# Kernel optimization log

Hardware: AMD Instinct MI355X
Metric: run time of the kernel (lower is better)

## Reference

```python
import jax, jax.numpy as jnp
import numpy as np

BATCH = 32768


def _unpack(packed, n):
    # packed: [rows, ceil(n/8)] ints in [0,256). Extract bits MSB-first per byte.
    bits = (packed[:, :, None] >> jnp.arange(7, -1, -1, dtype=packed.dtype)) & 1
    return bits.reshape(packed.shape[0], -1)[:, :n]  # [rows, n] of {0,1}


def setup_inputs() -> dict:
    key = jax.random.key(0)
    k0, k1, k2, k3, k4 = jax.random.split(key, 5)
    return {
        "x": jax.random.normal(k0, (BATCH, 784), dtype=jnp.float32),
        "w1_packed": jax.random.randint(k1, (256, 98), 0, 256, dtype=jnp.int32),
        "m1_packed": jax.random.randint(k2, (256, 98), 0, 256, dtype=jnp.int32),
        "alpha1": jnp.float32(1.0),
        "w2_packed": jax.random.randint(k3, (10, 32), 0, 256, dtype=jnp.int32),
        "m2_packed": jax.random.randint(k4, (10, 32), 0, 256, dtype=jnp.int32),
        "alpha2": jnp.float32(1.0),
    }


def reference(x, w1_packed, m1_packed, alpha1, w2_packed, m2_packed, alpha2):
    # Layer 1: binary {-1,+1} weights * {0,1} mask * alpha
    w1 = (2 * _unpack(w1_packed, 784) - 1).astype(jnp.float32)
    w1 = w1 * _unpack(m1_packed, 784).astype(jnp.float32) * alpha1  # [256, 784]
    h = jax.nn.relu(jnp.einsum('bi,oi->bo', x, w1))  # [B, 256]
    # Layer 2
    w2 = (2 * _unpack(w2_packed, 256) - 1).astype(jnp.float32)
    w2 = w2 * _unpack(m2_packed, 256).astype(jnp.float32) * alpha2  # [10, 256]
    return jnp.einsum('bh,oh->bo', h, w2)  # [B, 10]
```

## Files before the change

### kernel.cpp

```cpp
#include <hip/hip_runtime.h>
#include <hip/hip_bf16.h>

typedef __bf16 bf16x8 __attribute__((ext_vector_type(8)));
typedef float floatx4 __attribute__((ext_vector_type(4)));

#define GLB_AS __attribute__((address_space(1)))
#define LDS_AS __attribute__((address_space(3)))

__device__ __forceinline__ void async_cp16(const void* g, void* l) {
  __builtin_amdgcn_global_load_lds((GLB_AS void*)g, (LDS_AS void*)l, 16, 0, 0);
}

__device__ __forceinline__ unsigned short f2bf(float f) {
  __bf16 b = (__bf16)f;
  return __builtin_bit_cast(unsigned short, b);
}

__global__ void decode_w1_kernel(const int* __restrict__ w1p,
                                 const int* __restrict__ m1p,
                                 unsigned short* __restrict__ w1d) {
  int t = blockIdx.x * 256 + threadIdx.x;
  if (t >= 256 * 100) return;
  int r = t / 100;
  int j = t - r * 100;
  unsigned short vals[8];
#pragma unroll
  for (int k = 0; k < 8; ++k) vals[k] = 0;
  if (j < 98) {
    unsigned int v = (unsigned int)w1p[r * 98 + j];
    unsigned int m = (unsigned int)m1p[r * 98 + j];
#pragma unroll
    for (int k = 0; k < 8; ++k) {
      unsigned int bit = (v >> (7 - k)) & 1u;
      unsigned int mk  = (m >> (7 - k)) & 1u;
      vals[k] = (unsigned short)(mk ? (bit ? 0x3F80u : 0xBF80u) : 0u);
    }
  }
  uint4 pack;
  pack.x = (unsigned)vals[0] | ((unsigned)vals[1] << 16);
  pack.y = (unsigned)vals[2] | ((unsigned)vals[3] << 16);
  pack.z = (unsigned)vals[4] | ((unsigned)vals[5] << 16);
  pack.w = (unsigned)vals[6] | ((unsigned)vals[7] << 16);
  *reinterpret_cast<uint4*>(w1d + t * 8) = pack;
}

#define BM 64
#define BK 32
#define NCH 25
#define W1LD 800
#define HS_LD 264

__global__ __launch_bounds__(256, 2) void fused_kernel(
    const float* __restrict__ x,
    const unsigned short* __restrict__ w1d,
    const int* __restrict__ w2p,
    const int* __restrict__ m2p,
    const float* __restrict__ a1p,
    const float* __restrict__ a2p,
    float* __restrict__ out) {
  __shared__ unsigned short smem[64 * 264 + 16 * 256];

  const int tid  = threadIdx.x;
  const int wave = tid >> 6;
  const int lane = tid & 63;
  const int l15  = lane & 15;
  const int quad = lane >> 4;
  const int row0 = blockIdx.x * BM;

  const int OFF_XS = 0;
  const int OFF_WS = 2048;
  const int OFF_HS = 0;
  const int OFF_W2 = 16896;

  floatx4 acc[4][4];
#pragma unroll
  for (int i = 0; i < 4; ++i)
#pragma unroll
    for (int j = 0; j < 4; ++j) acc[i][j] = (floatx4){0.f, 0.f, 0.f, 0.f};

  for (int kc = 0; kc < NCH; ++kc) {
#pragma unroll
    for (int it = 0; it < 4; ++it) {
      int seg = it * 256 + tid;
      int r = seg >> 2, c = seg & 3;
      async_cp16(w1d + r * W1LD + kc * BK + c * 8, &smem[OFF_WS + seg * 8]);
    }
    float4 xv[2];
#pragma unroll
    for (int it = 0; it < 2; ++it) {
      int seg = it * 256 + tid;
      int r = seg >> 3, c4 = seg & 7;
      int col = kc * BK + c4 * 4;
      if (col < 784) {
        xv[it] = *reinterpret_cast<const float4*>(
            x + (size_t)(row0 + r) * 784 + col);
      } else {
        xv[it] = (float4){0.f, 0.f, 0.f, 0.f};
      }
    }
#pragma unroll
    for (int it = 0; it < 2; ++it) {
      int seg = it * 256 + tid;
      int r = seg >> 3, c4 = seg & 7;
      ushort4 b;
      b.x = f2bf(xv[it].x); b.y = f2bf(xv[it].y);
      b.z = f2bf(xv[it].z); b.w = f2bf(xv[it].w);
      *reinterpret_cast<ushort4*>(&smem[OFF_XS + r * BK + c4 * 4]) = b;
    }
    __syncthreads();

    bf16x8 af[4], bfr[4];
#pragma unroll
    for (int mi = 0; mi < 4; ++mi)
      af[mi] = *reinterpret_cast<const bf16x8*>(
          &smem[OFF_XS + (mi * 16 + l15) * BK + quad * 8]);
#pragma unroll
    for (int nj = 0; nj < 4; ++nj)
      bfr[nj] = *reinterpret_cast<const bf16x8*>(
          &smem[OFF_WS + (wave * 64 + nj * 16 + l15) * BK + quad * 8]);
#pragma unroll
    for (int mi = 0; mi < 4; ++mi)
#pragma unroll
      for (int nj = 0; nj < 4; ++nj)
        acc[mi][nj] = __builtin_amdgcn_mfma_f32_16x16x32_bf16(
            af[mi], bfr[nj], acc[mi][nj], 0, 0, 0);
    __syncthreads();
  }

  const float a1 = a1p[0];
  const float a2 = a2p[0];
#pragma unroll
  for (int mi = 0; mi < 4; ++mi) {
#pragma unroll
    for (int nj = 0; nj < 4; ++nj) {
      int col   = wave * 64 + nj * 16 + l15;
      int rbase = mi * 16 + quad * 4;
#pragma unroll
      for (int r = 0; r < 4; ++r) {
        float h = fmaxf(a1 * acc[mi][nj][r], 0.f);
        smem[OFF_HS + (rbase + r) * HS_LD + col] = f2bf(h);
      }
    }
  }
#pragma unroll
  for (int it = 0; it < 2; ++it) {
    int idx = it * 256 + tid;
    if (idx < 320) {
      int r = idx >> 5, j = idx & 31;
      unsigned int v = (unsigned int)w2p[r * 32 + j];
      unsigned int m = (unsigned int)m2p[r * 32 + j];
#pragma unroll
      for (int k = 0; k < 8; ++k) {
        unsigned int bit = (v >> (7 - k)) & 1u;
        unsigned int mk  = (m >> (7 - k)) & 1u;
        smem[OFF_W2 + r * 256 + j * 8 + k] =
            (unsigned short)(mk ? (bit ? 0x3F80u : 0xBF80u) : 0u);
      }
    }
  }
#pragma unroll
  for (int r = 10; r < 16; ++r) smem[OFF_W2 + r * 256 + tid] = 0;
  __syncthreads();

  floatx4 o2 = (floatx4){0.f, 0.f, 0.f, 0.f};
#pragma unroll
  for (int ks = 0; ks < 8; ++ks) {
    bf16x8 ha = *reinterpret_cast<const bf16x8*>(
        &smem[OFF_HS + (wave * 16 + l15) * HS_LD + ks * 32 + quad * 8]);
    bf16x8 wb = *reinterpret_cast<const bf16x8*>(
        &smem[OFF_W2 + l15 * 256 + ks * 32 + quad * 8]);
    o2 = __builtin_amdgcn_mfma_f32_16x16x32_bf16(ha, wb, o2, 0, 0, 0);
  }
  if (l15 < 10) {
#pragma unroll
    for (int r = 0; r < 4; ++r) {
      int gr = row0 + wave * 16 + quad * 4 + r;
      out[(size_t)gr * 10 + l15] = a2 * o2[r];
    }
  }
}

extern "C" void kernel_launch(void* const* d_in, const int* in_sizes, int n_in,
                              void* d_out, int out_size, void* d_ws, size_t ws_size,
                              hipStream_t stream) {
  const float* x   = (const float*)d_in[0];
  const int*   w1p = (const int*)d_in[1];
  const int*   m1p = (const int*)d_in[2];
  const float* a1  = (const float*)d_in[3];
  const int*   w2p = (const int*)d_in[4];
  const int*   m2p = (const int*)d_in[5];
  const float* a2  = (const float*)d_in[6];
  unsigned short* w1d = (unsigned short*)d_ws;
  float* out = (float*)d_out;

  decode_w1_kernel<<<100, 256, 0, stream>>>(w1p, m1p, w1d);
  fused_kernel<<<512, 256, 0, stream>>>(x, w1d, w2p, m2p, a1, a2, out);
}
```

Baseline: 187.5 us.

## Load MFMA fragments directly from global memory, drop LDS staging and barriers

The layer-1 GEMM no longer stages x and decoded W1 tiles through LDS with two barriers per K-chunk. Each wave now reads its A fragments (fp32 x, converted to bf16 in registers) and its B fragments (bf16 W1) straight from global memory, with x register-prefetched one chunk ahead. Waves are rearranged into a 2x2 grid, each owning 32 rows by 128 columns, so accumulators become 2x8 tiles. This removes LDS traffic and synchronisation, but W1 is re-read from global or L2 by every wave and the per-lane loads are strided, so it relies on cache hits.

```diff
diff --git a/kernel.cpp b/kernel.cpp
--- a/kernel.cpp
+++ b/kernel.cpp
@@ -3,13 +3,6 @@
 
 typedef __bf16 bf16x8 __attribute__((ext_vector_type(8)));
 typedef float floatx4 __attribute__((ext_vector_type(4)));
-
-#define GLB_AS __attribute__((address_space(1)))
-#define LDS_AS __attribute__((address_space(3)))
-
-__device__ __forceinline__ void async_cp16(const void* g, void* l) {
-  __builtin_amdgcn_global_load_lds((GLB_AS void*)g, (LDS_AS void*)l, 16, 0, 0);
-}
 
 __device__ __forceinline__ unsigned short f2bf(float f) {
   __bf16 b = (__bf16)f;
@@ -44,9 +37,6 @@
   *reinterpret_cast<uint4*>(w1d + t * 8) = pack;
 }
 
-#define BM 64
-#define BK 32
-#define NCH 25
 #define W1LD 800
 #define HS_LD 264
 
@@ -58,83 +48,96 @@
     const float* __restrict__ a1p,
     const float* __restrict__ a2p,
     float* __restrict__ out) {
-  __shared__ unsigned short smem[64 * 264 + 16 * 256];
+  __shared__ unsigned short smem[64 * HS_LD + 16 * 256];
 
   const int tid  = threadIdx.x;
   const int wave = tid >> 6;
   const int lane = tid & 63;
   const int l15  = lane & 15;
   const int quad = lane >> 4;
-  const int row0 = blockIdx.x * BM;
-
-  const int OFF_XS = 0;
-  const int OFF_WS = 2048;
+  const int wm   = wave >> 1;
+  const int wn   = wave & 1;
+  const int row0 = blockIdx.x * 64;
+
   const int OFF_HS = 0;
-  const int OFF_W2 = 16896;
-
-  floatx4 acc[4][4];
-#pragma unroll
-  for (int i = 0; i < 4; ++i)
-#pragma unroll
-    for (int j = 0; j < 4; ++j) acc[i][j] = (floatx4){0.f, 0.f, 0.f, 0.f};
-
-  for (int kc = 0; kc < NCH; ++kc) {
-#pragma unroll
-    for (int it = 0; it < 4; ++it) {
-      int seg = it * 256 + tid;
-      int r = seg >> 2, c = seg & 3;
-      async_cp16(w1d + r * W1LD + kc * BK + c * 8, &smem[OFF_WS + seg * 8]);
-    }
-    float4 xv[2];
-#pragma unroll
-    for (int it = 0; it < 2; ++it) {
-      int seg = it * 256 + tid;
-      int r = seg >> 3, c4 = seg & 7;
-      int col = kc * BK + c4 * 4;
-      if (col < 784) {
-        xv[it] = *reinterpret_cast<const float4*>(
-            x + (size_t)(row0 + r) * 784 + col);
+  const int OFF_W2 = 64 * HS_LD;
+
+  const float* xbase[2];
+#pragma unroll
+  for (int mi = 0; mi < 2; ++mi)
+    xbase[mi] = x + (size_t)(row0 + wm * 32 + mi * 16 + l15) * 784;
+  const unsigned short* wbase[8];
+#pragma unroll
+  for (int nj = 0; nj < 8; ++nj)
+    wbase[nj] = w1d + (size_t)(wn * 128 + nj * 16 + l15) * W1LD;
+
+  floatx4 acc[2][8];
+#pragma unroll
+  for (int i = 0; i < 2; ++i)
+#pragma unroll
+    for (int j = 0; j < 8; ++j) acc[i][j] = (floatx4){0.f, 0.f, 0.f, 0.f};
+
+  const float4 z4 = (float4){0.f, 0.f, 0.f, 0.f};
+
+  auto ldA = [&](int kc, float4 a[2][2]) {
+    int k = kc * 32 + quad * 8;
+    bool ok = (k < 784);
+#pragma unroll
+    for (int mi = 0; mi < 2; ++mi) {
+      if (ok) {
+        a[mi][0] = *reinterpret_cast<const float4*>(xbase[mi] + k);
+        a[mi][1] = *reinterpret_cast<const float4*>(xbase[mi] + k + 4);
       } else {
-        xv[it] = (float4){0.f, 0.f, 0.f, 0.f};
+        a[mi][0] = z4;
+        a[mi][1] = z4;
       }
     }
-#pragma unroll
-    for (int it = 0; it < 2; ++it) {
-      int seg = it * 256 + tid;
-      int r = seg >> 3, c4 = seg & 7;
-      ushort4 b;
-      b.x = f2bf(xv[it].x); b.y = f2bf(xv[it].y);
-      b.z = f2bf(xv[it].z); b.w = f2bf(xv[it].w);
-      *reinterpret_cast<ushort4*>(&smem[OFF_XS + r * BK + c4 * 4]) = b;
-    }
-    __syncthreads();
-
-    bf16x8 af[4], bfr[4];
-#pragma unroll
-    for (int mi = 0; mi < 4; ++mi)
-      af[mi] = *reinterpret_cast<const bf16x8*>(
-          &smem[OFF_XS + (mi * 16 + l15) * BK + quad * 8]);
-#pragma unroll
-    for (int nj = 0; nj < 4; ++nj)
-      bfr[nj] = *reinterpret_cast<const bf16x8*>(
-          &smem[OFF_WS + (wave * 64 + nj * 16 + l15) * BK + quad * 8]);
-#pragma unroll
-    for (int mi = 0; mi < 4; ++mi)
-#pragma unroll
-      for (int nj = 0; nj < 4; ++nj)
+  };
+
+  float4 cur[2][2], nxt[2][2];
+  ldA(0, cur);
+
+#pragma unroll 1
+  for (int kc = 0; kc < 25; ++kc) {
+    int kb = kc * 32 + quad * 8;
+    bf16x8 bfrag[8];
+#pragma unroll
+    for (int nj = 0; nj < 8; ++nj)
+      bfrag[nj] = *reinterpret_cast<const bf16x8*>(wbase[nj] + kb);
+    if (kc < 24) ldA(kc + 1, nxt);
+    bf16x8 afrag[2];
+#pragma unroll
+    for (int mi = 0; mi < 2; ++mi) {
+      afrag[mi][0] = (__bf16)cur[mi][0].x;
+      afrag[mi][1] = (__bf16)cur[mi][0].y;
+      afrag[mi][2] = (__bf16)cur[mi][0].z;
+      afrag[mi][3] = (__bf16)cur[mi][0].w;
+      afrag[mi][4] = (__bf16)cur[mi][1].x;
+      afrag[mi][5] = (__bf16)cur[mi][1].y;
+      afrag[mi][6] = (__bf16)cur[mi][1].z;
+      afrag[mi][7] = (__bf16)cur[mi][1].w;
+    }
+#pragma unroll
+    for (int mi = 0; mi < 2; ++mi)
+#pragma unroll
+      for (int nj = 0; nj < 8; ++nj)
         acc[mi][nj] = __builtin_amdgcn_mfma_f32_16x16x32_bf16(
-            af[mi], bfr[nj], acc[mi][nj], 0, 0, 0);
-    __syncthreads();
+            afrag[mi], bfrag[nj], acc[mi][nj], 0, 0, 0);
+#pragma unroll
+    for (int mi = 0; mi < 2; ++mi) {
+      cur[mi][0] = nxt[mi][0];
+      cur[mi][1] = nxt[mi][1];
+    }
   }
 
   const float a1 = a1p[0];
   const float a2 = a2p[0];
 #pragma unroll
-  for (int mi = 0; mi < 4; ++mi) {
-#pragma unroll
-    for (int nj = 0; nj < 4; ++nj) {
-      int col   = wave * 64 + nj * 16 + l15;
-      int rbase = mi * 16 + quad * 4;
+  for (int mi = 0; mi < 2; ++mi) {
+#pragma unroll
+    for (int nj = 0; nj < 8; ++nj) {
+      int col   = wn * 128 + nj * 16 + l15;
+      int rbase = wm * 32 + mi * 16 + quad * 4;
 #pragma unroll
       for (int r = 0; r < 4; ++r) {
         float h = fmaxf(a1 * acc[mi][nj][r], 0.f);
```

After: 205.0 us. 1.09x slower.

## Stage whole x slab in LDS and stream pre-tiled W1 fragments from global

Applied to the files above, without the earlier changes.

Each block now handles 32 rows and first loads that block's whole x slab (784 columns) into LDS as bf16, with padding, behind a single barrier. The per-chunk LDS staging of W1 and its two barriers per K step are removed; W1 is pre-laid out by the decode kernel into MFMA-fragment tiles and read straight from global/L2 into registers, double-buffered one chunk ahead. The grid doubles to 1024 blocks and the launch bound moves to 3 blocks per SM. In exchange, each block now re-reads the full W1 from cache, and only half the waves do the second layer.

```diff
diff --git a/kernel.cpp b/kernel.cpp
--- a/kernel.cpp
+++ b/kernel.cpp
@@ -3,13 +3,6 @@
 
 typedef __bf16 bf16x8 __attribute__((ext_vector_type(8)));
 typedef float floatx4 __attribute__((ext_vector_type(4)));
-
-#define GLB_AS __attribute__((address_space(1)))
-#define LDS_AS __attribute__((address_space(3)))
-
-__device__ __forceinline__ void async_cp16(const void* g, void* l) {
-  __builtin_amdgcn_global_load_lds((GLB_AS void*)g, (LDS_AS void*)l, 16, 0, 0);
-}
 
 __device__ __forceinline__ unsigned short f2bf(float f) {
   __bf16 b = (__bf16)f;
@@ -41,16 +34,17 @@
   pack.y = (unsigned)vals[2] | ((unsigned)vals[3] << 16);
   pack.z = (unsigned)vals[4] | ((unsigned)vals[5] << 16);
   pack.w = (unsigned)vals[6] | ((unsigned)vals[7] << 16);
-  *reinterpret_cast<uint4*>(w1d + t * 8) = pack;
+  int c0   = j * 8;
+  int off  = (((r >> 4) * 25 + (c0 >> 5)) << 9) + ((r & 15) << 5) + (c0 & 31);
+  *reinterpret_cast<uint4*>(w1d + off) = pack;
 }
 
-#define BM 64
-#define BK 32
-#define NCH 25
-#define W1LD 800
+#define W1TILE 12800
+#define SLAB_LD 808
 #define HS_LD 264
+#define OFF_W2 (32 * HS_LD)
 
-__global__ __launch_bounds__(256, 2) void fused_kernel(
+__global__ __launch_bounds__(256, 3) void fused_kernel(
     const float* __restrict__ x,
     const unsigned short* __restrict__ w1d,
     const int* __restrict__ w2p,
@@ -58,87 +52,86 @@
     const float* __restrict__ a1p,
     const float* __restrict__ a2p,
     float* __restrict__ out) {
-  __shared__ unsigned short smem[64 * 264 + 16 * 256];
+  __shared__ unsigned short smem[32 * SLAB_LD];
 
   const int tid  = threadIdx.x;
   const int wave = tid >> 6;
   const int lane = tid & 63;
   const int l15  = lane & 15;
   const int quad = lane >> 4;
-  const int row0 = blockIdx.x * BM;
+  const int row0 = blockIdx.x * 32;
 
-  const int OFF_XS = 0;
-  const int OFF_WS = 2048;
-  const int OFF_HS = 0;
-  const int OFF_W2 = 16896;
+  const float* xs = x + (size_t)row0 * 784;
+#pragma unroll
+  for (int i = 0; i < 25; ++i) {
+    int f = i * 256 + tid;
+    if (f < 6272) {
+      float4 v = *reinterpret_cast<const float4*>(xs + (size_t)f * 4);
+      int r = f / 196;
+      int c = (f - r * 196) * 4;
+      ushort4 b;
+      b.x = f2bf(v.x); b.y = f2bf(v.y); b.z = f2bf(v.z); b.w = f2bf(v.w);
+      *reinterpret_cast<ushort4*>(&smem[r * SLAB_LD + c]) = b;
+    }
+  }
+  if (tid < 128) {
+    int r = tid >> 2, g = tid & 3;
+    ushort4 z = {0, 0, 0, 0};
+    *reinterpret_cast<ushort4*>(&smem[r * SLAB_LD + 784 + g * 4]) = z;
+  }
+  __syncthreads();
 
-  floatx4 acc[4][4];
+  const unsigned short* wb[4];
 #pragma unroll
-  for (int i = 0; i < 4; ++i)
+  for (int nj = 0; nj < 4; ++nj)
+    wb[nj] = w1d + (size_t)(wave * 4 + nj) * W1TILE + l15 * 32 + quad * 8;
+
+  floatx4 acc[2][4];
+#pragma unroll
+  for (int i = 0; i < 2; ++i)
 #pragma unroll
     for (int j = 0; j < 4; ++j) acc[i][j] = (floatx4){0.f, 0.f, 0.f, 0.f};
 
-  for (int kc = 0; kc < NCH; ++kc) {
+  bf16x8 bcur[4], bnext[4];
 #pragma unroll
-    for (int it = 0; it < 4; ++it) {
-      int seg = it * 256 + tid;
-      int r = seg >> 2, c = seg & 3;
-      async_cp16(w1d + r * W1LD + kc * BK + c * 8, &smem[OFF_WS + seg * 8]);
-    }
-    float4 xv[2];
+  for (int nj = 0; nj < 4; ++nj)
+    bcur[nj] = *reinterpret_cast<const bf16x8*>(wb[nj]);
+
+#pragma unroll 1
+  for (int kc = 0; kc < 25; ++kc) {
+    int kn = (kc < 24) ? (kc + 1) : 24;
 #pragma unroll
-    for (int it = 0; it < 2; ++it) {
-      int seg = it * 256 + tid;
-      int r = seg >> 3, c4 = seg & 7;
-      int col = kc * BK + c4 * 4;
-      if (col < 784) {
-        xv[it] = *reinterpret_cast<const float4*>(
-            x + (size_t)(row0 + r) * 784 + col);
-      } else {
-        xv[it] = (float4){0.f, 0.f, 0.f, 0.f};
-      }
+    for (int nj = 0; nj < 4; ++nj)
+      bnext[nj] = *reinterpret_cast<const bf16x8*>(wb[nj] + kn * 512);
+    const int ko = kc * 32 + quad * 8;
+    bf16x8 a0 = *reinterpret_cast<const bf16x8*>(&smem[l15 * SLAB_LD + ko]);
+    bf16x8 a1 =
+        *reinterpret_cast<const bf16x8*>(&smem[(16 + l15) * SLAB_LD + ko]);
+#pragma unroll
+    for (int nj = 0; nj < 4; ++nj) {
+      acc[0][nj] = __builtin_amdgcn_mfma_f32_16x16x32_bf16(a0, bcur[nj],
+                                                           acc[0][nj], 0, 0, 0);
+      acc[1][nj] = __builtin_amdgcn_mfma_f32_16x16x32_bf16(a1, bcur[nj],
+                                                           acc[1][nj], 0, 0, 0);
     }
 #pragma unroll
-    for (int it = 0; it < 2; ++it) {
-      int seg = it * 256 + tid;
-      int r = seg >> 3, c4 = seg & 7;
-      ushort4 b;
-      b.x = f2bf(xv[it].x); b.y = f2bf(xv[it].y);
-      b.z = f2bf(xv[it].z); b.w = f2bf(xv[it].w);
-      *reinterpret_cast<ushort4*>(&smem[OFF_XS + r * BK + c4 * 4]) = b;
-    }
-    __syncthreads();
-
-    bf16x8 af[4], bfr[4];
-#pragma unroll
-    for (int mi = 0; mi < 4; ++mi)
-      af[mi] = *reinterpret_cast<const bf16x8*>(
-          &smem[OFF_XS + (mi * 16 + l15) * BK + quad * 8]);
-#pragma unroll
-    for (int nj = 0; nj < 4; ++nj)
-      bfr[nj] = *reinterpret_cast<const bf16x8*>(
-          &smem[OFF_WS + (wave * 64 + nj * 16 + l15) * BK + quad * 8]);
-#pragma unroll
-    for (int mi = 0; mi < 4; ++mi)
-#pragma unroll
-      for (int nj = 0; nj < 4; ++nj)
-        acc[mi][nj] = __builtin_amdgcn_mfma_f32_16x16x32_bf16(
-            af[mi], bfr[nj], acc[mi][nj], 0, 0, 0);
-    __syncthreads();
+    for (int nj = 0; nj < 4; ++nj) bcur[nj] = bnext[nj];
   }
 
-  const float a1 = a1p[0];
-  const float a2 = a2p[0];
+  __syncthreads();
+
+  const float a1s = a1p[0];
+  const float a2s = a2p[0];
 #pragma unroll
-  for (int mi = 0; mi < 4; ++mi) {
+  for (int mi = 0; mi < 2; ++mi) {
 #pragma unroll
     for (int nj = 0; nj < 4; ++nj) {
       int col   = wave * 64 + nj * 16 + l15;
       int rbase = mi * 16 + quad * 4;
 #pragma unroll
       for (int r = 0; r < 4; ++r) {
-        float h = fmaxf(a1 * acc[mi][nj][r], 0.f);
-        smem[OFF_HS + (rbase + r) * HS_LD + col] = f2bf(h);
+        float h = fmaxf(a1s * acc[mi][nj][r], 0.f);
+        smem[(rbase + r) * HS_LD + col] = f2bf(h);
       }
     }
   }
@@ -153,29 +146,31 @@
       for (int k = 0; k < 8; ++k) {
         unsigned int bit = (v >> (7 - k)) & 1u;
         unsigned int mk  = (m >> (7 - k)) & 1u;
-        smem[OFF_W2 + r * 256 + j * 8 + k] =
+        smem[OFF_W2 + r * HS_LD + j * 8 + k] =
             (unsigned short)(mk ? (bit ? 0x3F80u : 0xBF80u) : 0u);
       }
     }
   }
 #pragma unroll
-  for (int r = 10; r < 16; ++r) smem[OFF_W2 + r * 256 + tid] = 0;
+  for (int r = 10; r < 16; ++r) smem[OFF_W2 + r * HS_LD + tid] = 0;
   __syncthreads();
 
-  floatx4 o2 = (floatx4){0.f, 0.f, 0.f, 0.f};
+  if (wave < 2) {
+    floatx4 o2 = (floatx4){0.f, 0.f, 0.f, 0.f};
 #pragma unroll
-  for (int ks = 0; ks < 8; ++ks) {
-    bf16x8 ha = *reinterpret_cast<const bf16x8*>(
-        &smem[OFF_HS + (wave * 16 + l15) * HS_LD + ks * 32 + quad * 8]);
-    bf16x8 wb = *reinterpret_cast<const bf16x8*>(
-        &smem[OFF_W2 + l15 * 256 + ks * 32 + quad * 8]);
-    o2 = __builtin_amdgcn_mfma_f32_16x16x32_bf16(ha, wb, o2, 0, 0, 0);
-  }
-  if (l15 < 10) {
+    for (int ks = 0; ks < 8; ++ks) {
+      bf16x8 ha = *reinterpret_cast<const bf16x8*>(
+          &smem[(wave * 16 + l15) * HS_LD + ks * 32 + quad * 8]);
+      bf16x8 wv = *reinterpret_cast<const bf16x8*>(
+          &smem[OFF_W2 + l15 * HS_LD + ks * 32 + quad * 8]);
+      o2 = __builtin_amdgcn_mfma_f32_16x16x32_bf16(ha, wv, o2, 0, 0, 0);
+    }
+    if (l15 < 10) {
 #pragma unroll
-    for (int r = 0; r < 4; ++r) {
-      int gr = row0 + wave * 16 + quad * 4 + r;
-      out[(size_t)gr * 10 + l15] = a2 * o2[r];
+      for (int r = 0; r < 4; ++r) {
+        int gr = row0 + wave * 16 + quad * 4 + r;
+        out[(size_t)gr * 10 + l15] = a2s * o2[r];
+      }
     }
   }
 }
@@ -194,5 +189,5 @@
   float* out = (float*)d_out;
 
   decode_w1_kernel<<<100, 256, 0, stream>>>(w1p, m1p, w1d);
-  fused_kernel<<<512, 256, 0, stream>>>(x, w1d, w2p, m2p, a1, a2, out);
+  fused_kernel<<<1024, 256, 0, stream>>>(x, w1d, w2p, m2p, a1, a2, out);
 }
```

Measured after the change: 191.5 us. 1.02x slower.
